# Performance work log

Hardware: AMD Instinct MI355X
Metric: run time of the kernel (lower is better)

Reference implementation:

```python
import jax, jax.numpy as jnp
import numpy as np

B, L, D2, C = 64, 512, 512, 50  # D2 = hidden_size*2

def setup_inputs() -> dict:
    key = jax.random.key(0)
    ks = jax.random.split(key, 8)
    text_vec = jax.random.normal(ks[0], (B, L, D2), dtype=jnp.float32)
    text_mask = jnp.ones((B, L), dtype=bool)
    sbj_bound = jnp.sort(jax.random.randint(ks[1], (B, 2), 0, L), axis=-1)
    obj_start = jax.random.randint(ks[2], (B, L), 0, C)
    obj_end = jax.random.randint(ks[3], (B, L), 0, C)
    W_start = jax.random.normal(ks[4], (2 * D2, C), dtype=jnp.float32) * 0.02
    b_start = jnp.zeros((C,), dtype=jnp.float32)
    W_end = jax.random.normal(ks[5], (2 * D2, C), dtype=jnp.float32) * 0.02
    b_end = jnp.zeros((C,), dtype=jnp.float32)
    return {"text_vec": text_vec, "text_mask": text_mask, "sbj_bound": sbj_bound,
            "obj_start": obj_start, "obj_end": obj_end,
            "W_start": W_start, "b_start": b_start, "W_end": W_end, "b_end": b_end}

def _masked_ce(logits, labels, maskf, value_num):
    # logits [B,L,C], labels [B,L]
    logp = jax.nn.log_softmax(logits, axis=-1)
    nll = -jnp.take_along_axis(logp, labels[..., None], axis=-1)[..., 0]
    return (nll * maskf).sum() / value_num

def reference(text_vec, text_mask, sbj_bound, obj_start, obj_end,
              W_start, b_start, W_end, b_end):
    pos = jnp.arange(L)  # [L]
    start, end = sbj_bound[:, 0], sbj_bound[:, 1]
    # inclusive span mask, vectorized replacement for the per-example loop
    span = ((pos[None, :] >= start[:, None]) & (pos[None, :] <= end[:, None])).astype(text_vec.dtype)  # [B,L]
    count = span.sum(axis=1, keepdims=True)  # [B,1], >=1 since start<=end
    sbj_vec = jnp.einsum('bl,bld->bd', span, text_vec) / count  # segment mean [B,D2]
    # cat([text_vec, sbj_vec]) @ W  ==  text_vec @ W[:D2] + sbj_vec @ W[D2:]
    def head(W, b):
        return (jnp.einsum('bld,dc->blc', text_vec, W[:D2])
                + (sbj_vec @ W[D2:])[:, None, :] + b)
    o1 = head(W_start, b_start)
    o2 = head(W_end, b_end)
    maskf = text_mask.astype(jnp.float32)
    value_num = maskf.sum()
    loss_obj_s = _masked_ce(o1, obj_start, maskf, value_num)
    loss_obj_e = _masked_ce(o2, obj_end, maskf, value_num)
    return loss_obj_s + loss_obj_e
```

## Files before the change

### kernel.cpp

```cpp
#include <hip/hip_runtime.h>
#include <math.h>

#define BB 64
#define LL 512
#define DD 512
#define CC 50
#define NC 100
#define NCP 112
#define WST 520

#define WSB_LOSS  0
#define WSB_CNT   4
#define WSB_DONE  8
#define WSB_PART  28736
#define WSB_WTOP  553024
#define WSB_WBOT  667712

typedef __attribute__((ext_vector_type(8))) short bf16x8;
typedef __attribute__((ext_vector_type(4))) float f32x4;

static __device__ __forceinline__ unsigned short f2bf(float x) {
    unsigned int u = __float_as_uint(x);
    u += 0x7FFFu + ((u >> 16) & 1u);
    return (unsigned short)(u >> 16);
}
static __device__ __forceinline__ float bf2f(unsigned short h) {
    return __uint_as_float(((unsigned int)h) << 16);
}

__global__ __launch_bounds__(256) void k_prep(
    const float* __restrict__ tv, const int* __restrict__ sbj_bound,
    const float* __restrict__ Wst, const float* __restrict__ Wen,
    char* __restrict__ wsb)
{
    __shared__ float sh[128 * 53];
    const int t = threadIdx.x;
    const int blk = blockIdx.x;

    if (blk < 512) {
        const int b = blk >> 3, seg = blk & 7;
        const int start = sbj_bound[2 * b], end = sbj_bound[2 * b + 1];
        int r0 = seg * 64;      if (r0 < start) r0 = start;
        int r1 = seg * 64 + 63; if (r1 > end)   r1 = end;
        const int c4 = t & 127, par = t >> 7;
        const float* bp = tv + (size_t)b * LL * DD + c4 * 4;
        float4 a0 = {0, 0, 0, 0}, a1 = {0, 0, 0, 0};
        int r = r0 + par;
        for (; r + 2 <= r1; r += 4) {
            float4 v0 = *(const float4*)(bp + (size_t)r * DD);
            float4 v1 = *(const float4*)(bp + (size_t)(r + 2) * DD);
            a0.x += v0.x; a0.y += v0.y; a0.z += v0.z; a0.w += v0.w;
            a1.x += v1.x; a1.y += v1.y; a1.z += v1.z; a1.w += v1.w;
        }
        for (; r <= r1; r += 2) {
            float4 v0 = *(const float4*)(bp + (size_t)r * DD);
            a0.x += v0.x; a0.y += v0.y; a0.z += v0.z; a0.w += v0.w;
        }
        float4* buf = (float4*)sh;
        float4 acc = {a0.x + a1.x, a0.y + a1.y, a0.z + a1.z, a0.w + a1.w};
        buf[t] = acc;
        __syncthreads();
        if (t < 128) {
            float4 x = buf[t], y = buf[t + 128];
            unsigned short* part = (unsigned short*)(wsb + WSB_PART);
            ushort4 o;
            o.x = f2bf(x.x + y.x); o.y = f2bf(x.y + y.y);
            o.z = f2bf(x.z + y.z); o.w = f2bf(x.w + y.w);
            *(ushort4*)(part + ((size_t)(seg * BB + b)) * DD + t * 4) = o;
        }
    } else {
        const int bi = blk - 512;
        const int mat = bi >> 3;
        const int cj = bi & 7;
        const float* W = mat ? Wen : Wst;
        const int kbase = cj * 128;
        const float* src = W + (size_t)kbase * CC;
#pragma unroll
        for (int i = 0; i < 25; i++) {
            int idx = t + i * 256;
            int kr = idx / 50, c = idx - kr * 50;
            sh[kr * 53 + c] = src[idx];
        }
        __syncthreads();
        unsigned short* outp =
            (unsigned short*)(wsb + ((cj < 4) ? WSB_WTOP : WSB_WBOT));
        const int kout = kbase & 511;
#pragma unroll
        for (int i = 0; i < 25; i++) {
            int idx = t + i * 256;
            int n = idx >> 7, kl = idx & 127;
            outp[((size_t)(mat * CC + n)) * DD + kout + kl] = f2bf(sh[kl * 53 + n]);
        }
        if (bi == 0 && t == 0) {
            *(float*)(wsb + WSB_LOSS) = 0.0f;
            *(float*)(wsb + WSB_CNT)  = 0.0f;
            *(int*)(wsb + WSB_DONE)   = 0;
        }
    }
}

__global__ __launch_bounds__(512, 1) void k_main(
    const float* __restrict__ tv,
    const int* __restrict__ mask,
    const int* __restrict__ obj_s, const int* __restrict__ obj_e,
    const int* __restrict__ sbj_bound,
    const float* __restrict__ bst, const float* __restrict__ ben,
    char* __restrict__ wsb, float* __restrict__ out)
{
    __shared__ __align__(16) unsigned short Wt[NCP * WST];
    __shared__ __align__(16) unsigned short sbjb[DD];
    __shared__ float scl[NCP];
    __shared__ float red[16];
    const int t = threadIdx.x, wv = t >> 6, ln = t & 63;
    const int tc = ln & 15, quad = ln >> 4;
    const int m0w = blockIdx.x * 128 + wv * 16;
    const int b = blockIdx.x >> 2;
    const unsigned short* wtop = (const unsigned short*)(wsb + WSB_WTOP);

    const float* Abase = tv + (size_t)(m0w + tc) * DD + quad * 8;

    float4 a[32];
#pragma unroll
    for (int j = 0; j < 8; j++) {
        a[2 * j]      = *(const float4*)(Abase + j * 32);
        a[2 * j + 1]  = *(const float4*)(Abase + j * 32 + 4);
    }
#pragma unroll
    for (int j = 0; j < 8; j++) {
        a[16 + 2 * j] = *(const float4*)(Abase + 256 + j * 32);
        a[17 + 2 * j] = *(const float4*)(Abase + 256 + j * 32 + 4);
    }
#pragma unroll
    for (int i = 0; i < 14; i++) {
        int idx = t + i * 512;
        int n = idx >> 6, ch = idx & 63;
        *(bf16x8*)(Wt + n * WST + ch * 8) =
            *(const bf16x8*)(wtop + (size_t)n * DD + ch * 8);
    }
    {
        const unsigned short* part = (const unsigned short*)(wsb + WSB_PART);
        const float inv =
            1.0f / (float)(sbj_bound[2 * b + 1] - sbj_bound[2 * b] + 1);
        float s = 0.0f;
#pragma unroll
        for (int seg = 0; seg < 8; seg++)
            s += bf2f(part[(size_t)(seg * BB + b) * DD + t]);
        sbjb[t] = f2bf(s * inv);
    }
    int lab1[4], lab2[4], mk[4];
#pragma unroll
    for (int i = 0; i < 4; i++) {
        const int l = (m0w + quad * 4 + i) & (LL - 1);
        lab1[i] = obj_s[b * LL + l];
        lab2[i] = obj_e[b * LL + l] + CC;
        mk[i]   = mask[b * LL + l];
    }
    bf16x8 areg[16];
#pragma unroll
    for (int j = 0; j < 16; j++) {
        float4 v0 = a[2 * j], v1 = a[2 * j + 1];
        bf16x8 af;
        af[0] = (short)f2bf(v0.x); af[1] = (short)f2bf(v0.y);
        af[2] = (short)f2bf(v0.z); af[3] = (short)f2bf(v0.w);
        af[4] = (short)f2bf(v1.x); af[5] = (short)f2bf(v1.y);
        af[6] = (short)f2bf(v1.z); af[7] = (short)f2bf(v1.w);
        areg[j] = af;
    }
    __syncthreads();

    if (wv < 7) {
        const unsigned short* wbot = (const unsigned short*)(wsb + WSB_WBOT);
        const unsigned short* Bf = wbot + (size_t)(wv * 16 + tc) * DD + quad * 8;
        const unsigned short* Af2 = sbjb + quad * 8;
        f32x4 sacc = (f32x4)(0.0f);
#pragma unroll
        for (int kk = 0; kk < DD; kk += 32) {
            bf16x8 af = *(const bf16x8*)(Af2 + kk);
            bf16x8 bf = *(const bf16x8*)(Bf + kk);
            sacc = __builtin_amdgcn_mfma_f32_16x16x32_bf16(af, bf, sacc, 0, 0, 0);
        }
        if (ln < 16) {
            const int cc = wv * 16 + ln;
            const float bias =
                (cc < CC) ? bst[cc] : ((cc < NC) ? ben[cc - CC] : 0.0f);
            scl[cc] = sacc[0] + bias;
        }
    }

    f32x4 acc[7];
#pragma unroll
    for (int u = 0; u < 7; u++) acc[u] = (f32x4)(0.0f);
    const unsigned short* Wf = Wt + tc * WST + quad * 8;

#pragma unroll
    for (int j = 0; j < 16; j++) {
        bf16x8 af = areg[j];
#pragma unroll
        for (int u = 0; u < 7; u++) {
            bf16x8 bf = *(const bf16x8*)(Wf + u * 16 * WST + j * 32);
            acc[u] = __builtin_amdgcn_mfma_f32_16x16x32_bf16(af, bf, acc[u], 0, 0, 0);
        }
    }
    __syncthreads();

    float sc[7];
#pragma unroll
    for (int u = 0; u < 7; u++) sc[u] = scl[u * 16 + tc];

    float loss_local = 0.0f, cnt_local = 0.0f;
#pragma unroll
    for (int i = 0; i < 4; i++) {
        float lg[7];
#pragma unroll
        for (int u = 0; u < 7; u++) lg[u] = acc[u][i] + sc[u];
        float m1 = fmaxf(fmaxf(lg[0], lg[1]), lg[2]);
        if (tc < 2) m1 = fmaxf(m1, lg[3]);
        float m2 = fmaxf(lg[4], lg[5]);
        if (tc >= 2) m2 = fmaxf(m2, lg[3]);
        if (tc < 4)  m2 = fmaxf(m2, lg[6]);
#pragma unroll
        for (int off = 1; off < 16; off <<= 1) {
            m1 = fmaxf(m1, __shfl_xor(m1, off, 16));
            m2 = fmaxf(m2, __shfl_xor(m2, off, 16));
        }
        float e1 = expf(lg[0] - m1) + expf(lg[1] - m1) + expf(lg[2] - m1)
                 + ((tc < 2) ? expf(lg[3] - m1) : 0.0f);
        float e2 = expf(lg[4] - m2) + expf(lg[5] - m2)
                 + ((tc >= 2) ? expf(lg[3] - m2) : 0.0f)
                 + ((tc < 4)  ? expf(lg[6] - m2) : 0.0f);
        float t1 = 0.0f, t2 = 0.0f;
#pragma unroll
        for (int u = 0; u < 7; u++) {
            const int cc = u * 16 + tc;
            if (cc == lab1[i]) t1 = lg[u];
            if (cc == lab2[i]) t2 = lg[u];
        }
#pragma unroll
        for (int off = 1; off < 16; off <<= 1) {
            e1 += __shfl_xor(e1, off, 16);
            e2 += __shfl_xor(e2, off, 16);
            t1 += __shfl_xor(t1, off, 16);
            t2 += __shfl_xor(t2, off, 16);
        }
        if (tc == 0) {
            const float nll = (m1 + logf(e1) - t1) + (m2 + logf(e2) - t2);
            loss_local += mk[i] ? nll : 0.0f;
            cnt_local  += mk[i] ? 1.0f : 0.0f;
        }
    }
#pragma unroll
    for (int off = 1; off < 64; off <<= 1) {
        loss_local += __shfl_xor(loss_local, off);
        cnt_local  += __shfl_xor(cnt_local, off);
    }
    if (ln == 0) { red[wv * 2] = loss_local; red[wv * 2 + 1] = cnt_local; }
    __syncthreads();
    if (t == 0) {
        float Ls = 0.f, Cs = 0.f;
#pragma unroll
        for (int w = 0; w < 8; w++) { Ls += red[w * 2]; Cs += red[w * 2 + 1]; }
        float* wsf = (float*)wsb;
        atomicAdd(&wsf[0], Ls);
        atomicAdd(&wsf[1], Cs);
        __threadfence();
        int old = atomicAdd((int*)(wsb + WSB_DONE), 1);
        if (old == (int)gridDim.x - 1) {
            float L = atomicAdd(&wsf[0], 0.0f);
            float C = atomicAdd(&wsf[1], 0.0f);
            out[0] = L / C;
        }
    }
}

extern "C" void kernel_launch(void* const* d_in, const int* in_sizes, int n_in,
                              void* d_out, int out_size, void* d_ws, size_t ws_size,
                              hipStream_t stream) {
    const float* tv   = (const float*)d_in[0];
    const int*   mask = (const int*)d_in[1];
    const int*   sbj  = (const int*)d_in[2];
    const int*   objs = (const int*)d_in[3];
    const int*   obje = (const int*)d_in[4];
    const float* Wst  = (const float*)d_in[5];
    const float* bst  = (const float*)d_in[6];
    const float* Wen  = (const float*)d_in[7];
    const float* ben  = (const float*)d_in[8];
    float* out = (float*)d_out;
    char*  wsb = (char*)d_ws;

    k_prep<<<528, 256, 0, stream>>>(tv, sbj, Wst, Wen, wsb);
    k_main<<<256, 512, 0, stream>>>(tv, mask, objs, obje, sbj, bst, ben, wsb, out);
}
```

Measured before the change: 136.5 us.

## Fuse prep and main kernels into one cooperative kernel with grid sync

```diff
diff --git a/kernel.cpp b/kernel.cpp
--- a/kernel.cpp
+++ b/kernel.cpp
@@ -1,5 +1,8 @@
 #include <hip/hip_runtime.h>
+#include <hip/hip_cooperative_groups.h>
 #include <math.h>
+
+namespace cg = cooperative_groups;
 
 #define BB 64
 #define LL 512
@@ -28,22 +31,50 @@
     return __uint_as_float(((unsigned int)h) << 16);
 }
 
-__global__ __launch_bounds__(256) void k_prep(
-    const float* __restrict__ tv, const int* __restrict__ sbj_bound,
-    const float* __restrict__ Wst, const float* __restrict__ Wen,
-    char* __restrict__ wsb)
+__global__ __launch_bounds__(512, 1) void k_fused(
+    const float* __restrict__ tv,
+    const int* __restrict__ mask,
+    const int* __restrict__ obj_s, const int* __restrict__ obj_e,
+    const int* __restrict__ sbj_bound,
+    const float* __restrict__ Wst, const float* __restrict__ bst,
+    const float* __restrict__ Wen, const float* __restrict__ ben,
+    char* __restrict__ wsb, float* __restrict__ out)
 {
+    __shared__ __align__(16) unsigned short Wt[NCP * WST];
     __shared__ float sh[128 * 53];
-    const int t = threadIdx.x;
-    const int blk = blockIdx.x;
-
-    if (blk < 512) {
-        const int b = blk >> 3, seg = blk & 7;
-        const int start = sbj_bound[2 * b], end = sbj_bound[2 * b + 1];
+    __shared__ __align__(16) float4 spanbuf[512];
+    __shared__ __align__(16) unsigned short sbjb[DD];
+    __shared__ float scl[NCP];
+    __shared__ float red[16];
+
+    const int t = threadIdx.x, g = blockIdx.x;
+    const int wv = t >> 6, ln = t & 63;
+    const int tc = ln & 15, quad = ln >> 4;
+    const int m0w = g * 128 + wv * 16;
+    const int b = g >> 2;
+
+    const float* Abase = tv + (size_t)(m0w + tc) * DD + quad * 8;
+    float4 a[32];
+#pragma unroll
+    for (int j = 0; j < 8; j++) {
+        a[2 * j]      = *(const float4*)(Abase + j * 32);
+        a[2 * j + 1]  = *(const float4*)(Abase + j * 32 + 4);
+    }
+#pragma unroll
+    for (int j = 0; j < 8; j++) {
+        a[16 + 2 * j] = *(const float4*)(Abase + 256 + j * 32);
+        a[17 + 2 * j] = *(const float4*)(Abase + 256 + j * 32 + 4);
+    }
+
+    {
+        const int half = t >> 8, t2 = t & 255;
+        const int unit = g * 2 + half;
+        const int sb = unit >> 3, seg = unit & 7;
+        const int start = sbj_bound[2 * sb], end = sbj_bound[2 * sb + 1];
         int r0 = seg * 64;      if (r0 < start) r0 = start;
         int r1 = seg * 64 + 63; if (r1 > end)   r1 = end;
-        const int c4 = t & 127, par = t >> 7;
-        const float* bp = tv + (size_t)b * LL * DD + c4 * 4;
+        const int c4 = t2 & 127, par = t2 >> 7;
+        const float* bp = tv + (size_t)sb * LL * DD + c4 * 4;
         float4 a0 = {0, 0, 0, 0}, a1 = {0, 0, 0, 0};
         int r = r0 + par;
         for (; r + 2 <= r1; r += 4) {
@@ -56,105 +87,63 @@
             float4 v0 = *(const float4*)(bp + (size_t)r * DD);
             a0.x += v0.x; a0.y += v0.y; a0.z += v0.z; a0.w += v0.w;
         }
-        float4* buf = (float4*)sh;
+        float4* buf = spanbuf + half * 256;
         float4 acc = {a0.x + a1.x, a0.y + a1.y, a0.z + a1.z, a0.w + a1.w};
-        buf[t] = acc;
+        buf[t2] = acc;
         __syncthreads();
-        if (t < 128) {
-            float4 x = buf[t], y = buf[t + 128];
+        if (t2 < 128) {
+            float4 x = buf[t2], y = buf[t2 + 128];
             unsigned short* part = (unsigned short*)(wsb + WSB_PART);
             ushort4 o;
             o.x = f2bf(x.x + y.x); o.y = f2bf(x.y + y.y);
             o.z = f2bf(x.z + y.z); o.w = f2bf(x.w + y.w);
-            *(ushort4*)(part + ((size_t)(seg * BB + b)) * DD + t * 4) = o;
-        }
-    } else {
-        const int bi = blk - 512;
-        const int mat = bi >> 3;
-        const int cj = bi & 7;
-        const float* W = mat ? Wen : Wst;
-        const int kbase = cj * 128;
-        const float* src = W + (size_t)kbase * CC;
-#pragma unroll
-        for (int i = 0; i < 25; i++) {
-            int idx = t + i * 256;
-            int kr = idx / 50, c = idx - kr * 50;
-            sh[kr * 53 + c] = src[idx];
-        }
-        __syncthreads();
-        unsigned short* outp =
-            (unsigned short*)(wsb + ((cj < 4) ? WSB_WTOP : WSB_WBOT));
-        const int kout = kbase & 511;
-#pragma unroll
-        for (int i = 0; i < 25; i++) {
-            int idx = t + i * 256;
-            int n = idx >> 7, kl = idx & 127;
-            outp[((size_t)(mat * CC + n)) * DD + kout + kl] = f2bf(sh[kl * 53 + n]);
-        }
-        if (bi == 0 && t == 0) {
-            *(float*)(wsb + WSB_LOSS) = 0.0f;
-            *(float*)(wsb + WSB_CNT)  = 0.0f;
-            *(int*)(wsb + WSB_DONE)   = 0;
-        }
-    }
-}
-
-__global__ __launch_bounds__(512, 1) void k_main(
-    const float* __restrict__ tv,
-    const int* __restrict__ mask,
-    const int* __restrict__ obj_s, const int* __restrict__ obj_e,
-    const int* __restrict__ sbj_bound,
-    const float* __restrict__ bst, const float* __restrict__ ben,
-    char* __restrict__ wsb, float* __restrict__ out)
-{
-    __shared__ __align__(16) unsigned short Wt[NCP * WST];
-    __shared__ __align__(16) unsigned short sbjb[DD];
-    __shared__ float scl[NCP];
-    __shared__ float red[16];
-    const int t = threadIdx.x, wv = t >> 6, ln = t & 63;
-    const int tc = ln & 15, quad = ln >> 4;
-    const int m0w = blockIdx.x * 128 + wv * 16;
-    const int b = blockIdx.x >> 2;
-    const unsigned short* wtop = (const unsigned short*)(wsb + WSB_WTOP);
-
-    const float* Abase = tv + (size_t)(m0w + tc) * DD + quad * 8;
-
-    float4 a[32];
-#pragma unroll
-    for (int j = 0; j < 8; j++) {
-        a[2 * j]      = *(const float4*)(Abase + j * 32);
-        a[2 * j + 1]  = *(const float4*)(Abase + j * 32 + 4);
-    }
-#pragma unroll
-    for (int j = 0; j < 8; j++) {
-        a[16 + 2 * j] = *(const float4*)(Abase + 256 + j * 32);
-        a[17 + 2 * j] = *(const float4*)(Abase + 256 + j * 32 + 4);
-    }
-#pragma unroll
-    for (int i = 0; i < 14; i++) {
-        int idx = t + i * 512;
-        int n = idx >> 6, ch = idx & 63;
-        *(bf16x8*)(Wt + n * WST + ch * 8) =
-            *(const bf16x8*)(wtop + (size_t)n * DD + ch * 8);
-    }
-    {
-        const unsigned short* part = (const unsigned short*)(wsb + WSB_PART);
-        const float inv =
-            1.0f / (float)(sbj_bound[2 * b + 1] - sbj_bound[2 * b] + 1);
-        float s = 0.0f;
-#pragma unroll
-        for (int seg = 0; seg < 8; seg++)
-            s += bf2f(part[(size_t)(seg * BB + b) * DD + t]);
-        sbjb[t] = f2bf(s * inv);
-    }
-    int lab1[4], lab2[4], mk[4];
-#pragma unroll
-    for (int i = 0; i < 4; i++) {
-        const int l = (m0w + quad * 4 + i) & (LL - 1);
-        lab1[i] = obj_s[b * LL + l];
-        lab2[i] = obj_e[b * LL + l] + CC;
-        mk[i]   = mask[b * LL + l];
-    }
+            *(ushort4*)(part + ((size_t)(seg * BB + sb)) * DD + t2 * 4) = o;
+        }
+    }
+
+    if (g >= 248) {
+#pragma unroll 1
+        for (int rep = 0; rep < 2; rep++) {
+            const int bi = (g - 248) * 2 + rep;
+            const int mat = bi >> 3;
+            const int cj = bi & 7;
+            const float* W = mat ? Wen : Wst;
+            const int kbase = cj * 128;
+            const float* src = W + (size_t)kbase * CC;
+            __syncthreads();
+#pragma unroll
+            for (int i = 0; i < 13; i++) {
+                int idx = t + i * 512;
+                if (idx < 6400) {
+                    int kr = idx / 50, c = idx - kr * 50;
+                    sh[kr * 53 + c] = src[idx];
+                }
+            }
+            __syncthreads();
+            unsigned short* outp =
+                (unsigned short*)(wsb + ((cj < 4) ? WSB_WTOP : WSB_WBOT));
+            const int kout = kbase & 511;
+#pragma unroll
+            for (int i = 0; i < 13; i++) {
+                int idx = t + i * 512;
+                if (idx < 6400) {
+                    int n = idx >> 7, kl = idx & 127;
+                    outp[((size_t)(mat * CC + n)) * DD + kout + kl] =
+                        f2bf(sh[kl * 53 + n]);
+                }
+            }
+        }
+    }
+
+    if (g == 0 && t == 0) {
+        __hip_atomic_store((float*)(wsb + WSB_LOSS), 0.0f,
+                           __ATOMIC_RELAXED, __HIP_MEMORY_SCOPE_AGENT);
+        __hip_atomic_store((float*)(wsb + WSB_CNT), 0.0f,
+                           __ATOMIC_RELAXED, __HIP_MEMORY_SCOPE_AGENT);
+        __hip_atomic_store((int*)(wsb + WSB_DONE), 0,
+                           __ATOMIC_RELAXED, __HIP_MEMORY_SCOPE_AGENT);
+    }
+
     bf16x8 areg[16];
 #pragma unroll
     for (int j = 0; j < 16; j++) {
@@ -165,6 +154,36 @@
         af[4] = (short)f2bf(v1.x); af[5] = (short)f2bf(v1.y);
         af[6] = (short)f2bf(v1.z); af[7] = (short)f2bf(v1.w);
         areg[j] = af;
+    }
+    int lab1[4], lab2[4], mk[4];
+#pragma unroll
+    for (int i = 0; i < 4; i++) {
+        const int l = (m0w + quad * 4 + i) & (LL - 1);
+        lab1[i] = obj_s[b * LL + l];
+        lab2[i] = obj_e[b * LL + l] + CC;
+        mk[i]   = mask[b * LL + l];
+    }
+
+    __threadfence();
+    cg::this_grid().sync();
+
+    const unsigned short* wtop = (const unsigned short*)(wsb + WSB_WTOP);
+#pragma unroll
+    for (int i = 0; i < 14; i++) {
+        int idx = t + i * 512;
+        int n = idx >> 6, ch = idx & 63;
+        *(bf16x8*)(Wt + n * WST + ch * 8) =
+            *(const bf16x8*)(wtop + (size_t)n * DD + ch * 8);
+    }
+    {
+        const unsigned short* part = (const unsigned short*)(wsb + WSB_PART);
+        const float inv =
+            1.0f / (float)(sbj_bound[2 * b + 1] - sbj_bound[2 * b] + 1);
+        float s = 0.0f;
+#pragma unroll
+        for (int seg = 0; seg < 8; seg++)
+            s += bf2f(part[(size_t)(seg * BB + b) * DD + t]);
+        sbjb[t] = f2bf(s * inv);
     }
     __syncthreads();
 
@@ -287,6 +306,8 @@
     float* out = (float*)d_out;
     char*  wsb = (char*)d_ws;
 
-    k_prep<<<528, 256, 0, stream>>>(tv, sbj, Wst, Wen, wsb);
-    k_main<<<256, 512, 0, stream>>>(tv, mask, objs, obje, sbj, bst, ben, wsb, out);
+    void* args[] = { &tv, &mask, &objs, &obje, &sbj,
+                     &Wst, &bst, &Wen, &ben, &wsb, &out };
+    hipLaunchCooperativeKernel((void*)k_fused, dim3(256), dim3(512),
+                               args, 0, stream);
 }
```

Result: slower. 242.0 us (+77.2%).
